# Performance work log

Hardware: AMD Instinct MI355X
Metric: run time of the kernel (lower is better)

The kernel has to match this reference:

```python
import jax, jax.numpy as jnp
import numpy as np

EMBED_DIM = 1024
NUM_HEADS = 16
HEAD_DIM = EMBED_DIM // NUM_HEADS


def setup_inputs() -> dict:
    key = jax.random.key(0)
    ks = jax.random.split(key, 9)
    s = 1.0 / np.sqrt(EMBED_DIM)
    x = jax.random.normal(ks[0], (2, 2048, EMBED_DIM), dtype=jnp.float32)
    Wq = jax.random.uniform(ks[1], (EMBED_DIM, EMBED_DIM), jnp.float32, -s, s)
    bq = jax.random.uniform(ks[2], (EMBED_DIM,), jnp.float32, -s, s)
    Wk = jax.random.uniform(ks[3], (EMBED_DIM, EMBED_DIM), jnp.float32, -s, s)
    bk = jax.random.uniform(ks[4], (EMBED_DIM,), jnp.float32, -s, s)
    Wv = jax.random.uniform(ks[5], (EMBED_DIM, EMBED_DIM), jnp.float32, -s, s)
    bv = jax.random.uniform(ks[6], (EMBED_DIM,), jnp.float32, -s, s)
    Wo = jax.random.uniform(ks[7], (EMBED_DIM, EMBED_DIM), jnp.float32, -s, s)
    bo = jax.random.uniform(ks[8], (EMBED_DIM,), jnp.float32, -s, s)
    return {"x": x, "Wq": Wq, "bq": bq, "Wk": Wk, "bk": bk,
            "Wv": Wv, "bv": bv, "Wo": Wo, "bo": bo}


def reference(x, Wq, bq, Wk, bk, Wv, bv, Wo, bo):
    B, N, C = x.shape
    H, D = NUM_HEADS, HEAD_DIM
    # nn.Linear: y = x @ W.T + b; here W stored as [in, out] so y = x @ W + b
    def split_heads(y):
        return y.reshape(B, N, H, D).transpose(0, 2, 1, 3)  # [B,H,N,D]
    q = split_heads(x @ Wq + bq)
    k = split_heads(x @ Wk + bk)
    v = split_heads(x @ Wv + bv)
    scores = jnp.einsum('bhnd,bhmd->bhnm', q, k) / jnp.sqrt(jnp.float32(D)).astype(x.dtype)
    attn = jax.nn.softmax(scores, axis=-1)
    ctx = jnp.einsum('bhnm,bhmd->bhnd', attn, v)
    ctx = ctx.transpose(0, 2, 1, 3).reshape(B, N, C)
    return ctx @ Wo + bo
```

## Files before the change

### kernel.cpp

```cpp
#include <hip/hip_runtime.h>
#include <hip/hip_bf16.h>
#include <stdint.h>
#include <stddef.h>

using bf16 = __hip_bfloat16;
using bf16x8 = __attribute__((ext_vector_type(8))) short;
using f32x4  = __attribute__((ext_vector_type(4))) float;
using f32x16 = __attribute__((ext_vector_type(16))) float;
typedef unsigned int u32x2 __attribute__((ext_vector_type(2)));
typedef unsigned int u32x4 __attribute__((ext_vector_type(4)));

#define MFMA16(a, b, c) __builtin_amdgcn_mfma_f32_16x16x32_bf16((a), (b), (c), 0, 0, 0)
#define MFMA32(a, b, c) __builtin_amdgcn_mfma_f32_32x32x16_bf16((a), (b), (c), 0, 0, 0)

#define GLD16(g, l)                                                            \
  __builtin_amdgcn_global_load_lds(                                            \
      (const __attribute__((address_space(1))) void*)(g),                      \
      (__attribute__((address_space(3))) void*)(l), 16, 0, 0)

__device__ __forceinline__ float exp2_fast(float x) {
#if __has_builtin(__builtin_amdgcn_exp2f)
  return __builtin_amdgcn_exp2f(x);
#else
  return __expf(x * 0.69314718056f);
#endif
}

__device__ __forceinline__ float fmax3(float a, float b, float c) {
  return fmaxf(fmaxf(a, b), c);
}

__device__ __forceinline__ unsigned int cvtpk_bf16(float lo, float hi) {
  unsigned int r;
  asm("v_cvt_pk_bf16_f32 %0, %1, %2" : "=v"(r) : "v"(lo), "v"(hi));
  return r;
}

__device__ __forceinline__ void permswap(unsigned int& a, unsigned int& b, int hi) {
#if __has_builtin(__builtin_amdgcn_permlane32_swap)
  u32x2 r = __builtin_amdgcn_permlane32_swap(a, b, false, false);
  a = r.x;
  b = r.y;
#else
  unsigned int sa = __shfl_xor((unsigned int)a, 32, 64);
  unsigned int sb = __shfl_xor((unsigned int)b, 32, 64);
  unsigned int an = hi ? sb : a;
  unsigned int bn = hi ? b : sa;
  a = an; b = bn;
#endif
}


__global__ void convert_x(const float* __restrict__ x, bf16* __restrict__ out) {
  const int i = blockIdx.x * 256 + threadIdx.x;
  const float4 v = ((const float4*)x)[i];
  __hip_bfloat162* o2 = (__hip_bfloat162*)(out + (size_t)i * 4);
  o2[0] = __float22bfloat162_rn(make_float2(v.x, v.y));
  o2[1] = __float22bfloat162_rn(make_float2(v.z, v.w));
}

__global__ void convert_w(const float* __restrict__ W0, const float* __restrict__ W1,
                          const float* __restrict__ W2, const float* __restrict__ W3,
                          bf16* __restrict__ Wt) {
  __shared__ float t[32][33];
  const int bx = blockIdx.x;
  const int mat = bx >> 10;
  const float* W = (mat == 0) ? W0 : (mat == 1) ? W1 : (mat == 2) ? W2 : W3;
  const int rem = bx & 1023;
  const int k0 = (rem >> 5) * 32, n0 = (rem & 31) * 32;
  const int c = threadIdx.x & 31, r0 = (threadIdx.x >> 5) * 4;
#pragma unroll
  for (int i = 0; i < 4; ++i) {
    const int r = r0 + i;
    t[r][c] = W[(size_t)(k0 + r) * 1024 + n0 + c];
  }
  __syncthreads();
  bf16* dst = Wt + (size_t)mat * 1024 * 1024;
#pragma unroll
  for (int i = 0; i < 4; ++i) {
    const int rn = r0 + i;
    dst[(size_t)(n0 + rn) * 1024 + k0 + c] = __float2bfloat16(t[c][rn]);
  }
}

__global__ void concat_bias(const float* __restrict__ bq, const float* __restrict__ bk,
                            const float* __restrict__ bv, const float* __restrict__ bo,
                            float* __restrict__ dst) {
  const int i = blockIdx.x * 256 + threadIdx.x;
  const float* src = (i < 1024) ? bq : (i < 2048) ? bk : (i < 3072) ? bv : bo;
  dst[i] = src[i & 1023];
}

__global__ __launch_bounds__(512, 2)
void gemm_qkv(const bf16* __restrict__ A, const bf16* __restrict__ Bt,
              const float* __restrict__ bias,
              bf16* __restrict__ Qb, bf16* __restrict__ Kb, bf16* __restrict__ Vt) {
  __shared__ bf16 Ab[2][128 * 64];
  __shared__ bf16 Bb[2][384 * 64];
  const int tid = threadIdx.x;
  const int lane = tid & 63, w = tid >> 6;
  const int wr = w >> 2, wc = w & 3;
  const int lrow = lane & 15, lgk = lane >> 4;

  const int bid = blockIdx.x;
  const int xcd = bid & 7, i5 = bid >> 3;
  const int xr = xcd >> 1, xc = xcd & 1;
  const int bm = (xr * 8 + (i5 & 7)) * 128;
  const int bn = (xc * 4 + (i5 >> 3)) * 384;

  f32x4 acc[4][6] = {};

  auto stageA = [&](int b, int kt) {
#pragma unroll
    for (int v = 0; v < 2; ++v) {
      const int c = v * 512 + tid;
      const int r = c >> 3, j = c & 7;
      GLD16(A + (size_t)(bm + r) * 1024 + kt * 64 + ((j ^ (r & 7)) * 8),
            &Ab[b][c * 8]);
    }
  };
  auto stageB = [&](int b, int kt, int u) {
#pragma unroll
    for (int v = 0; v < 2; ++v) {
      const int cl = v * 512 + tid;
      const int r = u * 128 + (cl >> 3), j = cl & 7;
      GLD16(Bt + (size_t)(bn + r) * 1024 + kt * 64 + ((j ^ ((r & 7))) * 8),
            &Bb[b][(r * 8 + (j)) * 8]);
    }
  };

  auto readA = [&](int b, bf16x8 (&dst)[8]) {
#pragma unroll
    for (int mf = 0; mf < 4; ++mf)
#pragma unroll
      for (int kk = 0; kk < 2; ++kk) {
        const int r = wr * 64 + mf * 16 + lrow;
        const int s = (kk * 4 + lgk) ^ (r & 7);
        dst[mf * 2 + kk] = *(const bf16x8*)(&Ab[b][(r * 8 + s) * 8]);
      }
  };
  auto readB2 = [&](int b, int nf0, bf16x8 (&dst)[4]) {
#pragma unroll
    for (int nf = 0; nf < 2; ++nf)
#pragma unroll
      for (int kk = 0; kk < 2; ++kk) {
        const int r = wc * 96 + (nf0 + nf) * 16 + lrow;
        const int s = (kk * 4 + lgk) ^ (r & 7);
        dst[nf * 2 + kk] = *(const bf16x8*)(&Bb[b][(r * 8 + s) * 8]);
      }
  };

  stageA(0, 0);
  stageB(0, 0, 0);
  stageB(0, 0, 1);
  stageB(0, 0, 2);
  stageA(1, 1);
  asm volatile("s_waitcnt vmcnt(2)" ::: "memory");
  __builtin_amdgcn_s_barrier();

  bf16x8 a_[8], b01[4], b23[4], b45[4];

  for (int t = 0; t < 16; ++t) {
    const int b = t & 1, nb = b ^ 1;
    if (t < 15) {
      stageB(nb, t + 1, 0);
      stageB(nb, t + 1, 1);
    }
    readA(b, a_);
    readB2(b, 0, b01);
    asm volatile("s_waitcnt lgkmcnt(0)" ::: "memory");
    __builtin_amdgcn_sched_barrier(0);
    __builtin_amdgcn_s_setprio(1);
#pragma unroll
    for (int mf = 0; mf < 4; ++mf)
#pragma unroll
      for (int nf = 0; nf < 2; ++nf)
#pragma unroll
        for (int kk = 0; kk < 2; ++kk)
          acc[mf][nf] = MFMA16(a_[mf * 2 + kk], b01[nf * 2 + kk], acc[mf][nf]);
    __builtin_amdgcn_s_setprio(0);
    if (t < 15) stageB(nb, t + 1, 2);
    readB2(b, 2, b23);
    asm volatile("s_waitcnt lgkmcnt(0)" ::: "memory");
    __builtin_amdgcn_sched_barrier(0);
    __builtin_amdgcn_s_setprio(1);
#pragma unroll
    for (int mf = 0; mf < 4; ++mf)
#pragma unroll
      for (int nf = 0; nf < 2; ++nf)
#pragma unroll
        for (int kk = 0; kk < 2; ++kk)
          acc[mf][2 + nf] = MFMA16(a_[mf * 2 + kk], b23[nf * 2 + kk], acc[mf][2 + nf]);
    __builtin_amdgcn_s_setprio(0);
    readB2(b, 4, b45);
    asm volatile("s_waitcnt lgkmcnt(0)" ::: "memory");
    __builtin_amdgcn_sched_barrier(0);
    __builtin_amdgcn_s_barrier();
    if (t < 14) stageA(b, t + 2);
    __builtin_amdgcn_s_setprio(1);
#pragma unroll
    for (int mf = 0; mf < 4; ++mf)
#pragma unroll
      for (int nf = 0; nf < 2; ++nf)
#pragma unroll
        for (int kk = 0; kk < 2; ++kk)
          acc[mf][4 + nf] = MFMA16(a_[mf * 2 + kk], b45[nf * 2 + kk], acc[mf][4 + nf]);
    __builtin_amdgcn_s_setprio(0);
    if (t < 14)
      asm volatile("s_waitcnt vmcnt(2)" ::: "memory");
    else
      asm volatile("s_waitcnt vmcnt(0)" ::: "memory");
    __builtin_amdgcn_s_barrier();
  }

#pragma unroll
  for (int mf = 0; mf < 4; ++mf) {
#pragma unroll
    for (int nf = 0; nf < 6; ++nf) {
      const int col = bn + wc * 96 + nf * 16 + lrow;
      const float bv_ = bias[col];
      const int row0 = bm + wr * 64 + mf * 16 + lgk * 4;
      const int which = col >> 10;
      const int hd = col & 1023;
      const int h = hd >> 6, d = hd & 63;
      const int bb = row0 >> 11, t0 = row0 & 2047;
      const int bh = bb * 16 + h;
      if (which == 2) {
        uint2 pk;
        pk.x = cvtpk_bf16(acc[mf][nf][0] + bv_, acc[mf][nf][1] + bv_);
        pk.y = cvtpk_bf16(acc[mf][nf][2] + bv_, acc[mf][nf][3] + bv_);
        *(uint2*)(Vt + ((size_t)bh * 64 + d) * 2048 + t0) = pk;
      } else if (which == 0) {
#pragma unroll
        for (int j = 0; j < 4; ++j)
          Qb[((size_t)bh * 2048 + t0 + j) * 64 + d] =
              __float2bfloat16((acc[mf][nf][j] + bv_) * 0.18033688f);
      } else {
#pragma unroll
        for (int j = 0; j < 4; ++j)
          Kb[((size_t)bh * 2048 + t0 + j) * 64 + d] =
              __float2bfloat16(acc[mf][nf][j] + bv_);
      }
    }
  }
}

__global__ __launch_bounds__(256)
void gemm_o(const bf16* __restrict__ A, const bf16* __restrict__ Bt,
            const float* __restrict__ bias, float* __restrict__ Of, int K) {
  __shared__ bf16 As[3][128 * 32];
  __shared__ bf16 Bs[3][64 * 32];
  const int tid = threadIdx.x;
  const int lane = tid & 63, w = tid >> 6;
  const int wr = w >> 1, wc = w & 1;
  const int lrow = lane & 15, lgk = lane >> 4;
  const int bm = blockIdx.y * 128, bn = blockIdx.x * 64;
  f32x4 acc[4][2] = {};
  const bf16* Ab = A + (size_t)bm * K;
  const bf16* Bb = Bt + (size_t)bn * K;
  const int e0 = tid, e1 = 256 + tid;
  const int NT = K >> 5;

  auto stage = [&](int s, int k0) {
    GLD16(Ab + (size_t)(e0 >> 2) * K + k0 + (e0 & 3) * 8, &As[s][e0 * 8]);
    GLD16(Ab + (size_t)(e1 >> 2) * K + k0 + (e1 & 3) * 8, &As[s][e1 * 8]);
    GLD16(Bb + (size_t)(e0 >> 2) * K + k0 + (e0 & 3) * 8, &Bs[s][e0 * 8]);
  };

  stage(0, 0);
  stage(1, 32);
  int cur = 0, nxt = 2;
  for (int t = 0; t < NT; ++t) {
    if (t < NT - 1)
      asm volatile("s_waitcnt vmcnt(3)" ::: "memory");
    else
      asm volatile("s_waitcnt vmcnt(0)" ::: "memory");
    __builtin_amdgcn_s_barrier();
    if (t + 2 < NT) {
      stage(nxt, (t + 2) << 5);
      nxt = (nxt == 2) ? 0 : nxt + 1;
    }
    bf16x8 af[4], bfr[2];
#pragma unroll
    for (int m = 0; m < 4; ++m)
      af[m] = *(const bf16x8*)(&As[cur][(wr * 64 + m * 16 + lrow) * 32 + lgk * 8]);
#pragma unroll
    for (int n = 0; n < 2; ++n)
      bfr[n] = *(const bf16x8*)(&Bs[cur][(wc * 32 + n * 16 + lrow) * 32 + lgk * 8]);
#pragma unroll
    for (int m = 0; m < 4; ++m)
#pragma unroll
      for (int n = 0; n < 2; ++n)
        acc[m][n] = MFMA16(af[m], bfr[n], acc[m][n]);
    cur = (cur == 2) ? 0 : cur + 1;
  }

#pragma unroll
  for (int m = 0; m < 4; ++m) {
#pragma unroll
    for (int n = 0; n < 2; ++n) {
      const int col = bn + wc * 32 + n * 16 + lrow;
      const float bv_ = bias[col];
      const int row0 = bm + wr * 64 + m * 16 + lgk * 4;
#pragma unroll
      for (int j = 0; j < 4; ++j)
        Of[(size_t)(row0 + j) * 1024 + col] = acc[m][n][j] + bv_;
    }
  }
}

__global__ __launch_bounds__(256, 2)
void attn_kernel(const bf16* __restrict__ Q, const bf16* __restrict__ Kb,
                 const bf16* __restrict__ Vt, bf16* __restrict__ ctx) {
  __shared__ bf16 Kl[2][64 * 64];
  __shared__ bf16 Vl[2][64 * 64];

  const int tid = threadIdx.x, lane = tid & 63, w = tid >> 6;
  const int lo5 = lane & 31, hi = lane >> 5;

  const int bid = blockIdx.x;
  const int xcd = bid & 7, idx = bid >> 3;
  const int bh = (xcd << 2) | (idx >> 4);
  const int qt = idx & 15;
  const int q0 = qt * 128 + w * 32;

  const bf16* Qbh = Q + (size_t)bh * 2048 * 64;
  const bf16* Kbh = Kb + (size_t)bh * 2048 * 64;
  const bf16* Vbh = Vt + (size_t)bh * 64 * 2048;

  bf16x8 qf[4];
#pragma unroll
  for (int f = 0; f < 4; ++f)
    qf[f] = *(const bf16x8*)(Qbh + (size_t)(q0 + lo5) * 64 + f * 16 + hi * 8);

  f32x16 o0 = {}, o1 = {};
  float m2 = -1e30f;
  float lsum = 0.f;

  auto stage = [&](int buf, int kv) {
#pragma unroll
    for (int i = 0; i < 2; ++i) {
      const int c = (w * 2 + i) * 64 + lane;
      const int r = c >> 3, j = c & 7;
      const int js = (j ^ (r & 7)) * 8;
      GLD16(Kbh + (size_t)(kv + r) * 64 + js, &Kl[buf][c * 8]);
      GLD16(Vbh + (size_t)r * 2048 + kv + js, &Vl[buf][c * 8]);
    }
  };

  bf16x8 pa[4];

  auto softmax_pa = [&](f32x16& s0, f32x16& s1) {
    float r1[11];
#pragma unroll
    for (int i = 0; i < 5; ++i)
      r1[i] = fmax3(s0[3 * i], s0[3 * i + 1], s0[3 * i + 2]);
    r1[5] = fmax3(s0[15], s1[0], s1[1]);
#pragma unroll
    for (int i = 0; i < 4; ++i)
      r1[6 + i] = fmax3(s1[2 + 3 * i], s1[3 + 3 * i], s1[4 + 3 * i]);
    r1[10] = fmaxf(s1[14], s1[15]);
    float r2[4];
#pragma unroll
    for (int i = 0; i < 3; ++i) r2[i] = fmax3(r1[3 * i], r1[3 * i + 1], r1[3 * i + 2]);
    r2[3] = fmaxf(r1[9], r1[10]);
    const float pm = fmaxf(fmax3(r2[0], r2[1], r2[2]), r2[3]);
    if (!__all(pm <= m2 + 11.5416f)) {
      const float mx = fmaxf(pm, __shfl_xor(pm, 32, 64));
      const float mn = fmaxf(m2, mx);
      const float corr = exp2_fast(m2 - mn);
      m2 = mn;
      lsum *= corr;
#pragma unroll
      for (int j = 0; j < 16; ++j) { o0[j] *= corr; o1[j] *= corr; }
    }
#pragma unroll
    for (int j = 0; j < 16; ++j) s0[j] = exp2_fast(s0[j] - m2);
#pragma unroll
    for (int j = 0; j < 16; ++j) s1[j] = exp2_fast(s1[j] - m2);
    float a8[8];
#pragma unroll
    for (int j = 0; j < 8; ++j) a8[j] = (s0[j] + s0[j + 8]) + (s1[j] + s1[j + 8]);
    float a4[4];
#pragma unroll
    for (int j = 0; j < 4; ++j) a4[j] = a8[j] + a8[j + 4];
    lsum += (a4[0] + a4[1]) + (a4[2] + a4[3]);
#pragma unroll
    for (int ks = 0; ks < 4; ++ks) {
      const f32x16& s = (ks < 2) ? s0 : s1;
      const int b0 = (ks & 1) * 8;
      unsigned int a0 = cvtpk_bf16(s[b0 + 0], s[b0 + 1]);
      unsigned int c0 = cvtpk_bf16(s[b0 + 4], s[b0 + 5]);
      unsigned int a1 = cvtpk_bf16(s[b0 + 2], s[b0 + 3]);
      unsigned int c1 = cvtpk_bf16(s[b0 + 6], s[b0 + 7]);
      permswap(a0, c0, hi);
      permswap(a1, c1, hi);
      u32x4 tt;
      tt.x = a0; tt.y = a1; tt.z = c0; tt.w = c1;
      pa[ks] = __builtin_bit_cast(bf16x8, tt);
    }
  };

  f32x16 sA0, sA1, sB0, sB1;
  bf16x8 vfA[8], vfB[8];

  auto step = [&](int t, f32x16& sC0, f32x16& sC1, bf16x8 (&vfC)[8],
                  f32x16& sP0, f32x16& sP1, bf16x8 (&vfP)[8]) {
    const int cur = t & 1;
    const int kv = t << 6;
    if (t < 31) stage(cur ^ 1, kv + 64);
    if (t < 31)
      asm volatile("s_waitcnt vmcnt(4)" ::: "memory");
    else
      asm volatile("s_waitcnt vmcnt(0)" ::: "memory");
    __builtin_amdgcn_s_barrier();
    bf16x8 kf[8];
#pragma unroll
    for (int kt = 0; kt < 2; ++kt)
#pragma unroll
      for (int f = 0; f < 4; ++f) {
        const int r = kt * 32 + lo5;
        kf[kt * 4 + f] =
            *(const bf16x8*)(&Kl[cur][(r * 8 + (((f << 1) + hi) ^ (r & 7))) * 8]);
      }
#pragma unroll
    for (int dt = 0; dt < 2; ++dt)
#pragma unroll
      for (int ks = 0; ks < 4; ++ks) {
        const int r = dt * 32 + lo5;
        vfC[dt * 4 + ks] =
            *(const bf16x8*)(&Vl[cur][(r * 8 + (((ks << 1) + hi) ^ (r & 7))) * 8]);
      }
    if (t > 0) softmax_pa(sP0, sP1);
    asm volatile("s_waitcnt lgkmcnt(0)" ::: "memory");
    __builtin_amdgcn_sched_barrier(0);
    __builtin_amdgcn_s_barrier();
    __builtin_amdgcn_s_setprio(1);
    sC0 = f32x16{};
    sC1 = f32x16{};
#pragma unroll
    for (int f = 0; f < 4; ++f) sC0 = MFMA32(kf[f], qf[f], sC0);
#pragma unroll
    for (int f = 0; f < 4; ++f) sC1 = MFMA32(kf[4 + f], qf[f], sC1);
    if (t > 0) {
#pragma unroll
      for (int ks = 0; ks < 4; ++ks) {
        o0 = MFMA32(vfP[ks], pa[ks], o0);
        o1 = MFMA32(vfP[4 + ks], pa[ks], o1);
      }
    }
    __builtin_amdgcn_s_setprio(0);
  };

  stage(0, 0);

  step(0, sA0, sA1, vfA, sB0, sB1, vfB);
  for (int tt = 1; tt < 31; tt += 2) {
    step(tt, sB0, sB1, vfB, sA0, sA1, vfA);
    step(tt + 1, sA0, sA1, vfA, sB0, sB1, vfB);
  }
  step(31, sB0, sB1, vfB, sA0, sA1, vfA);

  softmax_pa(sB0, sB1);
#pragma unroll
  for (int ks = 0; ks < 4; ++ks) {
    o0 = MFMA32(vfB[ks], pa[ks], o0);
    o1 = MFMA32(vfB[4 + ks], pa[ks], o1);
  }

  lsum += __shfl_xor(lsum, 32, 64);
  const float inv = 1.f / lsum;
  const int b = bh >> 4, h = bh & 15;
  bf16* crow = ctx + (size_t)(b * 2048 + q0 + lo5) * 1024 + h * 64;
#pragma unroll
  for (int g = 0; g < 4; ++g) {
    uint2 pk0, pk1;
    pk0.x = cvtpk_bf16(o0[4 * g + 0] * inv, o0[4 * g + 1] * inv);
    pk0.y = cvtpk_bf16(o0[4 * g + 2] * inv, o0[4 * g + 3] * inv);
    pk1.x = cvtpk_bf16(o1[4 * g + 0] * inv, o1[4 * g + 1] * inv);
    pk1.y = cvtpk_bf16(o1[4 * g + 2] * inv, o1[4 * g + 3] * inv);
    *(uint2*)(crow + 8 * g + 4 * hi) = pk0;
    *(uint2*)(crow + 32 + 8 * g + 4 * hi) = pk1;
  }
}


extern "C" void kernel_launch(void* const* d_in, const int* in_sizes, int n_in,
                              void* d_out, int out_size, void* d_ws, size_t ws_size,
                              hipStream_t stream) {
  const float* x  = (const float*)d_in[0];
  const float* Wq = (const float*)d_in[1];
  const float* bq = (const float*)d_in[2];
  const float* Wk = (const float*)d_in[3];
  const float* bk = (const float*)d_in[4];
  const float* Wv = (const float*)d_in[5];
  const float* bv = (const float*)d_in[6];
  const float* Wo = (const float*)d_in[7];
  const float* bo = (const float*)d_in[8];
  float* out = (float*)d_out;

  char* ws = (char*)d_ws;
  bf16* xb  = (bf16*)(ws);
  bf16* Wt  = (bf16*)(ws + ((size_t)8 << 20));
  bf16* Qb  = (bf16*)(ws + ((size_t)16 << 20));
  bf16* Kb  = (bf16*)(ws + ((size_t)24 << 20));
  bf16* Vt  = (bf16*)(ws + ((size_t)32 << 20));
  bf16* ctx = (bf16*)(ws + ((size_t)40 << 20));
  float* ba = (float*)(ws + ((size_t)48 << 20));

  convert_x<<<dim3(4096), dim3(256), 0, stream>>>(x, xb);
  convert_w<<<dim3(4096), dim3(256), 0, stream>>>(Wq, Wk, Wv, Wo, Wt);
  concat_bias<<<dim3(16), dim3(256), 0, stream>>>(bq, bk, bv, bo, ba);

  gemm_qkv<<<dim3(256), dim3(512), 0, stream>>>(xb, Wt, ba, Qb, Kb, Vt);

  attn_kernel<<<dim3(512), dim3(256), 0, stream>>>(Qb, Kb, Vt, ctx);

  gemm_o<<<dim3(16, 32), dim3(256), 0, stream>>>(
      ctx, Wt + (size_t)3072 * 1024, ba + 3072, out, 1024);
}
```

Measured before the change: 122.1 us.

## Store K/V in MFMA fragment layout and load directly to registers in attention

```diff
diff --git a/kernel.cpp b/kernel.cpp
--- a/kernel.cpp
+++ b/kernel.cpp
@@ -94,7 +94,7 @@
 __global__ __launch_bounds__(512, 2)
 void gemm_qkv(const bf16* __restrict__ A, const bf16* __restrict__ Bt,
               const float* __restrict__ bias,
-              bf16* __restrict__ Qb, bf16* __restrict__ Kb, bf16* __restrict__ Vt) {
+              bf16* __restrict__ Qb, bf16* __restrict__ Kf, bf16* __restrict__ Vf) {
   __shared__ bf16 Ab[2][128 * 64];
   __shared__ bf16 Bb[2][384 * 64];
   const int tid = threadIdx.x;
@@ -225,21 +225,29 @@
       const int h = hd >> 6, d = hd & 63;
       const int bb = row0 >> 11, t0 = row0 & 2047;
       const int bh = bb * 16 + h;
+      const int tt = (t0 >> 6) & 31;
       if (which == 2) {
+        const int ks = (t0 >> 4) & 3, vhi = (t0 >> 3) & 1, e0 = t0 & 7;
+        const int dt = d >> 5, lo5 = d & 31;
+        bf16* vp = Vf + (((size_t)bh * 32 + tt) * 8 + dt * 4 + ks) * 512 +
+                   (vhi * 32 + lo5) * 8 + e0;
         uint2 pk;
         pk.x = cvtpk_bf16(acc[mf][nf][0] + bv_, acc[mf][nf][1] + bv_);
         pk.y = cvtpk_bf16(acc[mf][nf][2] + bv_, acc[mf][nf][3] + bv_);
-        *(uint2*)(Vt + ((size_t)bh * 64 + d) * 2048 + t0) = pk;
+        *(uint2*)vp = pk;
       } else if (which == 0) {
 #pragma unroll
         for (int j = 0; j < 4; ++j)
           Qb[((size_t)bh * 2048 + t0 + j) * 64 + d] =
               __float2bfloat16((acc[mf][nf][j] + bv_) * 0.18033688f);
       } else {
+        const int kt = (t0 >> 5) & 1, lo5 = t0 & 31;
+        const int f = d >> 4, khi = (d >> 3) & 1, e = d & 7;
+        bf16* kp = Kf + (((size_t)bh * 32 + tt) * 8 + kt * 4 + f) * 512 +
+                   (khi * 32 + lo5) * 8 + e;
 #pragma unroll
         for (int j = 0; j < 4; ++j)
-          Kb[((size_t)bh * 2048 + t0 + j) * 64 + d] =
-              __float2bfloat16(acc[mf][nf][j] + bv_);
+          kp[j * 8] = __float2bfloat16(acc[mf][nf][j] + bv_);
       }
     }
   }
@@ -310,11 +318,8 @@
 }
 
 __global__ __launch_bounds__(256, 2)
-void attn_kernel(const bf16* __restrict__ Q, const bf16* __restrict__ Kb,
-                 const bf16* __restrict__ Vt, bf16* __restrict__ ctx) {
-  __shared__ bf16 Kl[2][64 * 64];
-  __shared__ bf16 Vl[2][64 * 64];
-
+void attn_kernel(const bf16* __restrict__ Q, const bf16* __restrict__ Kf,
+                 const bf16* __restrict__ Vf, bf16* __restrict__ ctx) {
   const int tid = threadIdx.x, lane = tid & 63, w = tid >> 6;
   const int lo5 = lane & 31, hi = lane >> 5;
 
@@ -325,8 +330,8 @@
   const int q0 = qt * 128 + w * 32;
 
   const bf16* Qbh = Q + (size_t)bh * 2048 * 64;
-  const bf16* Kbh = Kb + (size_t)bh * 2048 * 64;
-  const bf16* Vbh = Vt + (size_t)bh * 64 * 2048;
+  const bf16* Kp = Kf + (size_t)bh * 32 * 4096 + lane * 8;
+  const bf16* Vp = Vf + (size_t)bh * 32 * 4096 + lane * 8;
 
   bf16x8 qf[4];
 #pragma unroll
@@ -336,18 +341,6 @@
   f32x16 o0 = {}, o1 = {};
   float m2 = -1e30f;
   float lsum = 0.f;
-
-  auto stage = [&](int buf, int kv) {
-#pragma unroll
-    for (int i = 0; i < 2; ++i) {
-      const int c = (w * 2 + i) * 64 + lane;
-      const int r = c >> 3, j = c & 7;
-      const int js = (j ^ (r & 7)) * 8;
-      GLD16(Kbh + (size_t)(kv + r) * 64 + js, &Kl[buf][c * 8]);
-      GLD16(Vbh + (size_t)r * 2048 + kv + js, &Vl[buf][c * 8]);
-    }
-  };
-
   bf16x8 pa[4];
 
   auto softmax_pa = [&](f32x16& s0, f32x16& s1) {
@@ -401,71 +394,40 @@
     }
   };
 
-  f32x16 sA0, sA1, sB0, sB1;
-  bf16x8 vfA[8], vfB[8];
-
-  auto step = [&](int t, f32x16& sC0, f32x16& sC1, bf16x8 (&vfC)[8],
-                  f32x16& sP0, f32x16& sP1, bf16x8 (&vfP)[8]) {
-    const int cur = t & 1;
-    const int kv = t << 6;
-    if (t < 31) stage(cur ^ 1, kv + 64);
-    if (t < 31)
-      asm volatile("s_waitcnt vmcnt(4)" ::: "memory");
-    else
-      asm volatile("s_waitcnt vmcnt(0)" ::: "memory");
-    __builtin_amdgcn_s_barrier();
-    bf16x8 kf[8];
-#pragma unroll
-    for (int kt = 0; kt < 2; ++kt)
-#pragma unroll
-      for (int f = 0; f < 4; ++f) {
-        const int r = kt * 32 + lo5;
-        kf[kt * 4 + f] =
-            *(const bf16x8*)(&Kl[cur][(r * 8 + (((f << 1) + hi) ^ (r & 7))) * 8]);
-      }
-#pragma unroll
-    for (int dt = 0; dt < 2; ++dt)
-#pragma unroll
-      for (int ks = 0; ks < 4; ++ks) {
-        const int r = dt * 32 + lo5;
-        vfC[dt * 4 + ks] =
-            *(const bf16x8*)(&Vl[cur][(r * 8 + (((ks << 1) + hi) ^ (r & 7))) * 8]);
-      }
-    if (t > 0) softmax_pa(sP0, sP1);
-    asm volatile("s_waitcnt lgkmcnt(0)" ::: "memory");
-    __builtin_amdgcn_sched_barrier(0);
-    __builtin_amdgcn_s_barrier();
-    __builtin_amdgcn_s_setprio(1);
-    sC0 = f32x16{};
-    sC1 = f32x16{};
-#pragma unroll
-    for (int f = 0; f < 4; ++f) sC0 = MFMA32(kf[f], qf[f], sC0);
-#pragma unroll
-    for (int f = 0; f < 4; ++f) sC1 = MFMA32(kf[4 + f], qf[f], sC1);
-    if (t > 0) {
-#pragma unroll
-      for (int ks = 0; ks < 4; ++ks) {
-        o0 = MFMA32(vfP[ks], pa[ks], o0);
-        o1 = MFMA32(vfP[4 + ks], pa[ks], o1);
-      }
-    }
-    __builtin_amdgcn_s_setprio(0);
-  };
-
-  stage(0, 0);
-
-  step(0, sA0, sA1, vfA, sB0, sB1, vfB);
-  for (int tt = 1; tt < 31; tt += 2) {
-    step(tt, sB0, sB1, vfB, sA0, sA1, vfA);
-    step(tt + 1, sA0, sA1, vfA, sB0, sB1, vfB);
-  }
-  step(31, sB0, sB1, vfB, sA0, sA1, vfA);
-
-  softmax_pa(sB0, sB1);
-#pragma unroll
-  for (int ks = 0; ks < 4; ++ks) {
-    o0 = MFMA32(vfB[ks], pa[ks], o0);
-    o1 = MFMA32(vfB[4 + ks], pa[ks], o1);
+  bf16x8 kA[8], kB[8], vb[8];
+
+  auto loadK = [&](int t, bf16x8 (&kb)[8]) {
+    const bf16* p = Kp + (size_t)t * 4096;
+#pragma unroll
+    for (int fi = 0; fi < 8; ++fi) kb[fi] = *(const bf16x8*)(p + fi * 512);
+  };
+  auto loadV = [&](int t) {
+    const bf16* p = Vp + (size_t)t * 4096;
+#pragma unroll
+    for (int fi = 0; fi < 8; ++fi) vb[fi] = *(const bf16x8*)(p + fi * 512);
+  };
+
+  loadK(0, kA);
+
+  auto step = [&](int t, bf16x8 (&kc)[8], bf16x8 (&kn)[8]) {
+    loadV(t);
+    if (t < 31) loadK(t + 1, kn);
+    f32x16 s0 = {}, s1 = {};
+#pragma unroll
+    for (int f = 0; f < 4; ++f) s0 = MFMA32(kc[f], qf[f], s0);
+#pragma unroll
+    for (int f = 0; f < 4; ++f) s1 = MFMA32(kc[4 + f], qf[f], s1);
+    softmax_pa(s0, s1);
+#pragma unroll
+    for (int ks = 0; ks < 4; ++ks) {
+      o0 = MFMA32(vb[ks], pa[ks], o0);
+      o1 = MFMA32(vb[4 + ks], pa[ks], o1);
+    }
+  };
+
+  for (int t = 0; t < 32; t += 2) {
+    step(t, kA, kB);
+    step(t + 1, kB, kA);
   }
 
   lsum += __shfl_xor(lsum, 32, 64);
@@ -503,8 +465,8 @@
   bf16* xb  = (bf16*)(ws);
   bf16* Wt  = (bf16*)(ws + ((size_t)8 << 20));
   bf16* Qb  = (bf16*)(ws + ((size_t)16 << 20));
-  bf16* Kb  = (bf16*)(ws + ((size_t)24 << 20));
-  bf16* Vt  = (bf16*)(ws + ((size_t)32 << 20));
+  bf16* Kf  = (bf16*)(ws + ((size_t)24 << 20));
+  bf16* Vf  = (bf16*)(ws + ((size_t)32 << 20));
   bf16* ctx = (bf16*)(ws + ((size_t)40 << 20));
   float* ba = (float*)(ws + ((size_t)48 << 20));
 
@@ -512,9 +474,9 @@
   convert_w<<<dim3(4096), dim3(256), 0, stream>>>(Wq, Wk, Wv, Wo, Wt);
   concat_bias<<<dim3(16), dim3(256), 0, stream>>>(bq, bk, bv, bo, ba);
 
-  gemm_qkv<<<dim3(256), dim3(512), 0, stream>>>(xb, Wt, ba, Qb, Kb, Vt);
-
-  attn_kernel<<<dim3(512), dim3(256), 0, stream>>>(Qb, Kb, Vt, ctx);
+  gemm_qkv<<<dim3(256), dim3(512), 0, stream>>>(xb, Wt, ba, Qb, Kf, Vf);
+
+  attn_kernel<<<dim3(512), dim3(256), 0, stream>>>(Qb, Kf, Vf, ctx);
 
   gemm_o<<<dim3(16, 32), dim3(256), 0, stream>>>(
       ctx, Wt + (size_t)3072 * 1024, ba + 3072, out, 1024);
```

Measured after the change: 122.8 us. No clear change (+0.6%).
